# Performance work log

Measured on AMD Instinct MI355X. Metric: run time of the kernel, lower is better.

Reference implementation:

```python
import jax, jax.numpy as jnp
import numpy as np

LN_EPS = 1e-5


def setup_inputs() -> dict:
    key = jax.random.key(0)
    ks = jax.random.split(key, 6)
    n_nodes, mem_dim = 500000, 256
    n_upd, msg_dim = 65536, 512
    return {
        "unique_node_ids": jnp.arange(n_upd, dtype=jnp.int64) if jax.config.jax_enable_x64 else jnp.arange(n_upd, dtype=jnp.int32),
        "unique_messages": jax.random.normal(ks[0], (n_upd, msg_dim), dtype=jnp.float32),
        "timestamps": jax.random.uniform(ks[1], (n_upd,), dtype=jnp.float32),
        "memory": jax.random.normal(ks[2], (n_nodes, mem_dim), dtype=jnp.float32),
        "last_update": jnp.zeros((n_nodes,), dtype=jnp.float32),
        "W_ih": jax.random.normal(ks[3], (3 * mem_dim, msg_dim), dtype=jnp.float32) * (1.0 / np.sqrt(msg_dim)),
        "W_hh": jax.random.normal(ks[4], (3 * mem_dim, mem_dim), dtype=jnp.float32) * (1.0 / np.sqrt(mem_dim)),
        "b_ih": jnp.zeros((3 * mem_dim,), dtype=jnp.float32),
        "b_hh": jnp.zeros((3 * mem_dim,), dtype=jnp.float32),
        "ln_gamma": jnp.ones((mem_dim,), dtype=jnp.float32),
        "ln_beta": jnp.zeros((mem_dim,), dtype=jnp.float32),
    }


def _gru_cell(x, h, W_ih, W_hh, b_ih, b_hh):
    # torch.nn.GRUCell math
    gi = x @ W_ih.T + b_ih          # [N, 3H]
    gh = h @ W_hh.T + b_hh          # [N, 3H]
    i_r, i_z, i_n = jnp.split(gi, 3, axis=-1)
    h_r, h_z, h_n = jnp.split(gh, 3, axis=-1)
    r = jax.nn.sigmoid(i_r + h_r)
    z = jax.nn.sigmoid(i_z + h_z)
    n = jnp.tanh(i_n + r * h_n)
    return (1.0 - z) * n + z * h


def _layer_norm(x, gamma, beta):
    mu = jnp.mean(x, axis=-1, keepdims=True)
    var = jnp.mean(jnp.square(x - mu), axis=-1, keepdims=True)
    return (x - mu) * jax.lax.rsqrt(var + LN_EPS) * gamma + beta


def reference(unique_node_ids, unique_messages, timestamps, memory, last_update,
              W_ih, W_hh, b_ih, b_hh, ln_gamma, ln_beta):
    # gather memory rows for the nodes being updated
    h = memory[unique_node_ids]                      # [N, H]
    new_h = _gru_cell(unique_messages, h, W_ih, W_hh, b_ih, b_hh)
    new_h = _layer_norm(new_h, ln_gamma, ln_beta)
    # scatter updated rows back (get_updated_memory semantics: pure copy)
    updated_memory = memory.at[unique_node_ids].set(new_h)
    updated_last_update = last_update.at[unique_node_ids].set(timestamps)
    return updated_memory, updated_last_update
```

## Files before the change

kernel.cpp:

```cpp
#include <hip/hip_runtime.h>
#include <hip/hip_bf16.h>

typedef float  f32x4 __attribute__((ext_vector_type(4)));
typedef short  s16x8 __attribute__((ext_vector_type(8)));

#define MEMH   256
#define MSGD   512
#define G3     768
#define W_IH_ELEMS (G3*MSGD)
#define W_HH_ELEMS (G3*MEMH)
#define W_TOT_ELEMS (W_IH_ELEMS + W_HH_ELEMS)
#define W_BYTES    ((size_t)W_TOT_ELEMS * 2)

#define BM     64
#define NTHR   1024
#define AH_OFF 0
#define AM_OFF 32768
#define O_OFF  32768
#define LDS_BYTES (32768 + 66560)

static __device__ __forceinline__ short f2bf(float x) {
    __hip_bfloat16 b = __float2bfloat16(x);
    return __builtin_bit_cast(short, b);
}
static __device__ __forceinline__ float bf2f(short s) {
    unsigned int u = ((unsigned int)(unsigned short)s) << 16;
    return __builtin_bit_cast(float, u);
}
static __device__ __forceinline__ float sigf(float x) {
    return 1.f / (1.f + __expf(-x));
}
static __device__ __forceinline__ float tanh_fast(float x) {
    float e = __expf(-2.f * fabsf(x));
    float t = (1.f - e) / (1.f + e);
    return copysignf(t, x);
}
static __device__ __forceinline__ f32x4 ntload4(const float* p) {
    return __builtin_nontemporal_load((const f32x4*)p);
}
static __device__ __forceinline__ void ntstore4(float* p, f32x4 v) {
    __builtin_nontemporal_store(v, (f32x4*)p);
}

__global__ void smu_copy_kernel(const float* __restrict__ mem,
                                const float* __restrict__ lu,
                                float* __restrict__ out_mem,
                                float* __restrict__ out_lu,
                                long n_mem4, long n_lu4) {
    long i = (long)blockIdx.x * blockDim.x + threadIdx.x;
    long stride = (long)gridDim.x * blockDim.x;
    long total = n_mem4 + n_lu4;
    for (; i < total; i += stride) {
        if (i < n_mem4) ntstore4(out_mem + i * 4, ntload4(mem + i * 4));
        else {
            long j = (i - n_mem4) * 4;
            ntstore4(out_lu + j, ntload4(lu + j));
        }
    }
}

__global__ void smu_cvtw_kernel(const float* __restrict__ wih,
                                const float* __restrict__ whh,
                                short* __restrict__ o) {
    int i = blockIdx.x * blockDim.x + threadIdx.x;
    if (i >= W_TOT_ELEMS) return;
    if (i < W_IH_ELEMS) {
        int f = i >> 9, r = i & 511, l = r >> 3, e = r & 7;
        int t = f >> 4, k = f & 15;
        int row = t * 16 + (l & 15), col = k * 32 + (l >> 4) * 8 + e;
        o[i] = f2bf(wih[row * MSGD + col]);
    } else {
        int j = i - W_IH_ELEMS;
        int f = j >> 9, r = j & 511, l = r >> 3, e = r & 7;
        int t = f >> 3, k = f & 7;
        int row = t * 16 + (l & 15), col = k * 32 + (l >> 4) * 8 + e;
        o[i] = f2bf(whh[row * MEMH + col]);
    }
}

__global__ void smu_bits_kernel(const int* __restrict__ ids,
                                unsigned* __restrict__ bm, int n) {
    int i = blockIdx.x * blockDim.x + threadIdx.x;
    if (i < n) {
        int id = ids[i];
        atomicOr(&bm[id >> 5], 1u << (id & 31));
    }
}

template<bool USE_WS>
static __device__ __forceinline__ s16x8 load_b(const float* __restrict__ Wf,
                                               const short* __restrict__ Wb,
                                               int t, int k, int ldk, int nkt, int lane) {
    if constexpr (USE_WS) {
        return *(const s16x8*)(Wb + ((size_t)(t * nkt + k) << 9) + lane * 8);
    } else {
        int row = t * 16 + (lane & 15);
        int col = k * 32 + (lane >> 4) * 8;
        f32x4 x = *(const f32x4*)(Wf + (size_t)row * ldk + col);
        f32x4 y = *(const f32x4*)(Wf + (size_t)row * ldk + col + 4);
        s16x8 s;
        s[0]=f2bf(x[0]); s[1]=f2bf(x[1]); s[2]=f2bf(x[2]); s[3]=f2bf(x[3]);
        s[4]=f2bf(y[0]); s[5]=f2bf(y[1]); s[6]=f2bf(y[2]); s[7]=f2bf(y[3]);
        return s;
    }
}

#define CP_LOAD(BUF, s) do { if constexpr (FUSED) {                                   \
    const int lo_ = (s) * 2;                                                          \
    const long o0_ = (long)w * 48 + lo_;                                              \
    const long r0_ = crow_base + o0_;                                                 \
    cpf_##BUF##0 = (o0_ < cpslab) && (r0_ < n_nodes) && !((cpwin >> lo_) & 1);        \
    cpf_##BUF##1 = (o0_ + 1 < cpslab) && (r0_ + 1 < n_nodes) && !((cpwin >> (lo_ + 1)) & 1); \
    if (cpf_##BUF##0) cpv_##BUF##0 = ntload4(memory + r0_ * MEMH + (lane << 2));      \
    if (cpf_##BUF##1) cpv_##BUF##1 = ntload4(memory + (r0_ + 1) * MEMH + (lane << 2));\
  } } while (0)

#define CP_STORE(BUF, s) do { if constexpr (FUSED) {                                  \
    const long r0_ = crow_base + (long)w * 48 + (s) * 2;                              \
    if (cpf_##BUF##0) ntstore4(out_mem + r0_ * MEMH + (lane << 2), cpv_##BUF##0);     \
    if (cpf_##BUF##1) ntstore4(out_mem + (r0_ + 1) * MEMH + (lane << 2), cpv_##BUF##1);\
    cpf_##BUF##0 = false; cpf_##BUF##1 = false;                                       \
  } } while (0)

template<bool USE_WS, bool FUSED>
__global__ __launch_bounds__(NTHR, 1)
void smu_gru_kernel(const int*   __restrict__ ids,
                    const float* __restrict__ msg,
                    const float* __restrict__ ts,
                    const float* __restrict__ memory,
                    const float* __restrict__ lu,
                    const float* __restrict__ W_ih,
                    const float* __restrict__ W_hh,
                    const float* __restrict__ b_ih,
                    const float* __restrict__ b_hh,
                    const float* __restrict__ gamma,
                    const float* __restrict__ beta,
                    const short* __restrict__ wsw,
                    const unsigned* __restrict__ bm,
                    float* __restrict__ out_mem,
                    float* __restrict__ out_lu,
                    long n_nodes, long cpslab) {
    __shared__ __align__(16) unsigned char lds[LDS_BYTES];
    const int tid  = threadIdx.x;
    const int bid  = blockIdx.x;
    const long base = (long)bid * BM;
    const long crow_base = (long)bid * cpslab;

    {
        const float* src = msg + base * MSGD;
        #pragma unroll
        for (int it = 0; it < 4; ++it) {
            int u = tid + NTHR * it;
            int row = u >> 6;
            f32x4 a = ntload4(src + u * 8);
            f32x4 b = ntload4(src + u * 8 + 4);
            s16x8 s;
            s[0]=f2bf(a[0]); s[1]=f2bf(a[1]); s[2]=f2bf(a[2]); s[3]=f2bf(a[3]);
            s[4]=f2bf(b[0]); s[5]=f2bf(b[1]); s[6]=f2bf(b[2]); s[7]=f2bf(b[3]);
            int byte = AM_OFF + ((u * 16) ^ ((row & 7) << 4));
            *(s16x8*)(lds + byte) = s;
        }
        #pragma unroll
        for (int it = 0; it < 2; ++it) {
            int u = tid + NTHR * it;
            int row = u >> 5;
            int c8  = u & 31;
            int id  = ids[base + row];
            const float* hs = memory + (size_t)id * MEMH + c8 * 8;
            f32x4 a = ntload4(hs);
            f32x4 b = ntload4(hs + 4);
            s16x8 s;
            s[0]=f2bf(a[0]); s[1]=f2bf(a[1]); s[2]=f2bf(a[2]); s[3]=f2bf(a[3]);
            s[4]=f2bf(b[0]); s[5]=f2bf(b[1]); s[6]=f2bf(b[2]); s[7]=f2bf(b[3]);
            int byte = AH_OFF + ((u * 16) ^ ((row & 7) << 4));
            *(s16x8*)(lds + byte) = s;
        }
    }
    __syncthreads();

    const int lane = tid & 63;
    const int w    = tid >> 6;
    const int lr   = lane & 15;
    const int lk8  = (lane >> 4) * 8;
    const int sw   = (lr & 7) << 4;
    const short* Wi = wsw;
    const short* Wh = wsw + W_IH_ELEMS;

    f32x4 cpv_A0, cpv_A1, cpv_B0, cpv_B1;
    bool  cpf_A0 = false, cpf_A1 = false, cpf_B0 = false, cpf_B1 = false;
    unsigned long long cpwin = 0;
    if constexpr (FUSED) {
        long start = crow_base + (long)w * 48;
        long wi = start >> 5;
        int  off = (int)(start & 31);
        unsigned b0 = bm[wi], b1 = bm[wi + 1], b2 = bm[wi + 2];
        unsigned long long lo64 = ((unsigned long long)b1 << 32) | b0;
        cpwin = lo64 >> off;
        if (off) cpwin |= ((unsigned long long)b2) << (64 - off);
    }

    f32x4 acc[4][3] = {};
    f32x4 accn[4]   = {};

    {
        s16x8 b[2][3];
        #pragma unroll
        for (int i = 0; i < 3; ++i) b[0][i] = load_b<USE_WS>(W_ih, Wi, w + 16*i, 0, MSGD, 16, lane);
        #pragma unroll
        for (int i = 0; i < 3; ++i) b[1][i] = load_b<USE_WS>(W_ih, Wi, w + 16*i, 1, MSGD, 16, lane);
        #pragma unroll
        for (int k = 0; k < 16; ++k) {
            if ((k & 1) == 0) { CP_STORE(A, k - 2); CP_LOAD(A, k); }
            else              { CP_STORE(B, k - 2); CP_LOAD(B, k); }
            const int cb = (k * 32 + lk8) * 2;
            #pragma unroll
            for (int m = 0; m < 4; ++m) {
                s16x8 a = *(const s16x8*)(lds + AM_OFF + (((m*16 + lr) * 1024 + cb) ^ sw));
                #pragma unroll
                for (int i = 0; i < 3; ++i)
                    acc[m][i] = __builtin_amdgcn_mfma_f32_16x16x32_bf16(a, b[k & 1][i], acc[m][i], 0, 0, 0);
            }
            if (k < 14) {
                #pragma unroll
                for (int i = 0; i < 3; ++i)
                    b[k & 1][i] = load_b<USE_WS>(W_ih, Wi, w + 16*i, k + 2, MSGD, 16, lane);
            }
        }
    }
    {
        s16x8 b[2][3];
        #pragma unroll
        for (int i = 0; i < 3; ++i) b[0][i] = load_b<USE_WS>(W_hh, Wh, w + 16*i, 0, MEMH, 8, lane);
        #pragma unroll
        for (int i = 0; i < 3; ++i) b[1][i] = load_b<USE_WS>(W_hh, Wh, w + 16*i, 1, MEMH, 8, lane);
        #pragma unroll
        for (int k = 0; k < 8; ++k) {
            if ((k & 1) == 0) { CP_STORE(A, 14 + k); CP_LOAD(A, 16 + k); }
            else              { CP_STORE(B, 14 + k); CP_LOAD(B, 16 + k); }
            const int cb = (k * 32 + lk8) * 2;
            #pragma unroll
            for (int m = 0; m < 4; ++m) {
                s16x8 a = *(const s16x8*)(lds + AH_OFF + (((m*16 + lr) * 512 + cb) ^ sw));
                acc[m][0] = __builtin_amdgcn_mfma_f32_16x16x32_bf16(a, b[k & 1][0], acc[m][0], 0, 0, 0);
                acc[m][1] = __builtin_amdgcn_mfma_f32_16x16x32_bf16(a, b[k & 1][1], acc[m][1], 0, 0, 0);
                accn[m]   = __builtin_amdgcn_mfma_f32_16x16x32_bf16(a, b[k & 1][2], accn[m],   0, 0, 0);
            }
            if (k < 6) {
                #pragma unroll
                for (int i = 0; i < 3; ++i)
                    b[k & 1][i] = load_b<USE_WS>(W_hh, Wh, w + 16*i, k + 2, MEMH, 8, lane);
            }
        }
    }
    CP_STORE(A, 22);
    CP_STORE(B, 23);

    __syncthreads();

    {
        const int lq = (lane >> 4) * 4;
        const int j  = w * 16 + lr;
        const float br = b_ih[j]       + b_hh[j];
        const float bz = b_ih[256 + j] + b_hh[256 + j];
        const float bihn = b_ih[512 + j], bhhn = b_hh[512 + j];
        #pragma unroll
        for (int m = 0; m < 4; ++m) {
            #pragma unroll
            for (int q = 0; q < 4; ++q) {
                int row = m * 16 + lq + q;
                float r = sigf(acc[m][0][q] + br);
                float z = sigf(acc[m][1][q] + bz);
                float n = tanh_fast(acc[m][2][q] + bihn + r * (accn[m][q] + bhhn));
                float hv = bf2f(*(const short*)(lds + AH_OFF + ((row * 512 + j * 2) ^ ((row & 7) << 4))));
                float o = (1.f - z) * n + z * hv;
                *(float*)(lds + O_OFF + (row * 260 + j) * 4) = o;
            }
        }
    }
    __syncthreads();

    #pragma unroll
    for (int rr = 0; rr < 4; ++rr) {
        int row = w * 4 + rr;
        f32x4 x = *(const f32x4*)(lds + O_OFF + (row * 260 + lane * 4) * 4);
        float s1 = x[0] + x[1] + x[2] + x[3];
        float s2 = x[0]*x[0] + x[1]*x[1] + x[2]*x[2] + x[3]*x[3];
        #pragma unroll
        for (int mm = 32; mm > 0; mm >>= 1) {
            s1 += __shfl_xor(s1, mm);
            s2 += __shfl_xor(s2, mm);
        }
        float mu  = s1 * (1.f / 256.f);
        float var = fmaxf(s2 * (1.f / 256.f) - mu * mu, 0.f);
        float inv = rsqrtf(var + 1e-5f);
        f32x4 g  = *(const f32x4*)(gamma + lane * 4);
        f32x4 be = *(const f32x4*)(beta  + lane * 4);
        int id = ids[base + row];
        f32x4 y;
        #pragma unroll
        for (int c = 0; c < 4; ++c) y[c] = (x[c] - mu) * inv * g[c] + be[c];
        ntstore4(out_mem + (size_t)id * MEMH + lane * 4, y);
        if (lane == 0) __builtin_nontemporal_store(ts[base + row], out_lu + id);
    }

    if constexpr (FUSED) {
        for (long o = 768 + w; o < cpslab; o += 16) {
            long row = crow_base + o;
            if (row < n_nodes && !((bm[row >> 5] >> (row & 31)) & 1u)) {
                f32x4 v = ntload4(memory + row * MEMH + (lane << 2));
                ntstore4(out_mem + row * MEMH + (lane << 2), v);
            }
        }
        for (long i = (long)bid * NTHR + tid; i < n_nodes; i += (long)gridDim.x * NTHR) {
            if (!((bm[i >> 5] >> (i & 31)) & 1u)) {
                float v = __builtin_nontemporal_load(lu + i);
                __builtin_nontemporal_store(v, out_lu + i);
            }
        }
    }
}

extern "C" void kernel_launch(void* const* d_in, const int* in_sizes, int n_in,
                              void* d_out, int out_size, void* d_ws, size_t ws_size,
                              hipStream_t stream) {
    (void)n_in; (void)out_size;
    const int*   ids = (const int*)  d_in[0];
    const float* msg = (const float*)d_in[1];
    const float* ts  = (const float*)d_in[2];
    const float* mem = (const float*)d_in[3];
    const float* lu  = (const float*)d_in[4];
    const float* Wih = (const float*)d_in[5];
    const float* Whh = (const float*)d_in[6];
    const float* bih = (const float*)d_in[7];
    const float* bhh = (const float*)d_in[8];
    const float* gam = (const float*)d_in[9];
    const float* bet = (const float*)d_in[10];

    const int  n_upd   = in_sizes[0];
    const long n_nodes = (long)in_sizes[3] / MEMH;

    float* out_mem = (float*)d_out;
    float* out_lu  = out_mem + (size_t)n_nodes * MEMH;

    const size_t bm_words = (size_t)((n_nodes + 31) / 32);
    const size_t bm_bytes_pad = bm_words * 4 + 16;
    const bool ws_w  = (d_ws != nullptr) && (ws_size >= W_BYTES);
    const bool ws_bm = (d_ws != nullptr) && (ws_size >= W_BYTES + bm_bytes_pad);

    short*    wsw = (short*)d_ws;
    unsigned* bm  = (unsigned*)((char*)d_ws + W_BYTES);

    if (ws_w) {
        smu_cvtw_kernel<<<(W_TOT_ELEMS + 255) / 256, 256, 0, stream>>>(Wih, Whh, wsw);
    }
    if (ws_bm) {
        (void)hipMemsetAsync(bm, 0, bm_bytes_pad, stream);
        smu_bits_kernel<<<(n_upd + 255) / 256, 256, 0, stream>>>(ids, bm, n_upd);
    }

    const int  grid   = n_upd / BM;
    const long cpslab = (n_nodes + grid - 1) / grid;

    if (ws_bm) {
        smu_gru_kernel<true, true><<<grid, NTHR, 0, stream>>>(
            ids, msg, ts, mem, lu, Wih, Whh, bih, bhh, gam, bet,
            wsw, bm, out_mem, out_lu, n_nodes, cpslab);
    } else {
        long n_mem4 = n_nodes * (MEMH / 4);
        long n_lu4  = n_nodes / 4;
        smu_copy_kernel<<<2048, 256, 0, stream>>>(mem, lu, out_mem, out_lu,
                                                  n_mem4, n_lu4);
        if (ws_w) {
            smu_gru_kernel<true, false><<<grid, NTHR, 0, stream>>>(
                ids, msg, ts, mem, lu, Wih, Whh, bih, bhh, gam, bet,
                wsw, nullptr, out_mem, out_lu, n_nodes, cpslab);
        } else {
            smu_gru_kernel<false, false><<<grid, NTHR, 0, stream>>>(
                ids, msg, ts, mem, lu, Wih, Whh, bih, bhh, gam, bet,
                nullptr, nullptr, out_mem, out_lu, n_nodes, cpslab);
        }
    }
}
```

Before: 386.3 us.

## Split bitmap-skipping memory copy out of GRU kernel into separate launch

Removes the copy of untouched memory rows that was interleaved with the MFMA loops inside the GRU kernel. That copy now runs in a dedicated grid-stride kernel, launched after the GRU kernel, which skips rows flagged in the update bitmap and issues four independent loads before storing. This simplifies the GRU kernel and may lower its register pressure. The cost is losing the overlap between compute and the roughly 500 MB streaming copy, plus one extra launch.

```diff
diff --git a/kernel.cpp b/kernel.cpp
--- a/kernel.cpp
+++ b/kernel.cpp
@@ -55,6 +55,54 @@
         else {
             long j = (i - n_mem4) * 4;
             ntstore4(out_lu + j, ntload4(lu + j));
+        }
+    }
+}
+
+__global__ __launch_bounds__(256)
+void smu_copy_skip_kernel(const float* __restrict__ mem,
+                          const float* __restrict__ lu,
+                          const unsigned* __restrict__ bm,
+                          float* __restrict__ out_mem,
+                          float* __restrict__ out_lu,
+                          long n_nodes) {
+    const long nu = n_nodes * (MEMH / 4);
+    const long stride = (long)gridDim.x * blockDim.x;
+    const long i0 = (long)blockIdx.x * blockDim.x + threadIdx.x;
+
+    for (long i = i0; i < nu; i += stride * 4) {
+        long  u0 = i, u1 = i + stride, u2 = i + stride * 2, u3 = i + stride * 3;
+        f32x4 v0, v1, v2, v3;
+        bool  f0 = false, f1 = false, f2 = false, f3 = false;
+        {
+            long r = u0 >> 6;
+            f0 = !((bm[r >> 5] >> (r & 31)) & 1u);
+            if (f0) v0 = ntload4(mem + u0 * 4);
+        }
+        if (u1 < nu) {
+            long r = u1 >> 6;
+            f1 = !((bm[r >> 5] >> (r & 31)) & 1u);
+            if (f1) v1 = ntload4(mem + u1 * 4);
+        }
+        if (u2 < nu) {
+            long r = u2 >> 6;
+            f2 = !((bm[r >> 5] >> (r & 31)) & 1u);
+            if (f2) v2 = ntload4(mem + u2 * 4);
+        }
+        if (u3 < nu) {
+            long r = u3 >> 6;
+            f3 = !((bm[r >> 5] >> (r & 31)) & 1u);
+            if (f3) v3 = ntload4(mem + u3 * 4);
+        }
+        if (f0) ntstore4(out_mem + u0 * 4, v0);
+        if (f1) ntstore4(out_mem + u1 * 4, v1);
+        if (f2) ntstore4(out_mem + u2 * 4, v2);
+        if (f3) ntstore4(out_mem + u3 * 4, v3);
+    }
+    for (long i = i0; i < n_nodes; i += stride) {
+        if (!((bm[i >> 5] >> (i & 31)) & 1u)) {
+            float v = __builtin_nontemporal_load(lu + i);
+            __builtin_nontemporal_store(v, out_lu + i);
         }
     }
 }
@@ -105,30 +153,12 @@
     }
 }
 
-#define CP_LOAD(BUF, s) do { if constexpr (FUSED) {                                   \
-    const int lo_ = (s) * 2;                                                          \
-    const long o0_ = (long)w * 48 + lo_;                                              \
-    const long r0_ = crow_base + o0_;                                                 \
-    cpf_##BUF##0 = (o0_ < cpslab) && (r0_ < n_nodes) && !((cpwin >> lo_) & 1);        \
-    cpf_##BUF##1 = (o0_ + 1 < cpslab) && (r0_ + 1 < n_nodes) && !((cpwin >> (lo_ + 1)) & 1); \
-    if (cpf_##BUF##0) cpv_##BUF##0 = ntload4(memory + r0_ * MEMH + (lane << 2));      \
-    if (cpf_##BUF##1) cpv_##BUF##1 = ntload4(memory + (r0_ + 1) * MEMH + (lane << 2));\
-  } } while (0)
-
-#define CP_STORE(BUF, s) do { if constexpr (FUSED) {                                  \
-    const long r0_ = crow_base + (long)w * 48 + (s) * 2;                              \
-    if (cpf_##BUF##0) ntstore4(out_mem + r0_ * MEMH + (lane << 2), cpv_##BUF##0);     \
-    if (cpf_##BUF##1) ntstore4(out_mem + (r0_ + 1) * MEMH + (lane << 2), cpv_##BUF##1);\
-    cpf_##BUF##0 = false; cpf_##BUF##1 = false;                                       \
-  } } while (0)
-
-template<bool USE_WS, bool FUSED>
+template<bool USE_WS>
 __global__ __launch_bounds__(NTHR, 1)
 void smu_gru_kernel(const int*   __restrict__ ids,
                     const float* __restrict__ msg,
                     const float* __restrict__ ts,
                     const float* __restrict__ memory,
-                    const float* __restrict__ lu,
                     const float* __restrict__ W_ih,
                     const float* __restrict__ W_hh,
                     const float* __restrict__ b_ih,
@@ -136,15 +166,12 @@
                     const float* __restrict__ gamma,
                     const float* __restrict__ beta,
                     const short* __restrict__ wsw,
-                    const unsigned* __restrict__ bm,
                     float* __restrict__ out_mem,
-                    float* __restrict__ out_lu,
-                    long n_nodes, long cpslab) {
+                    float* __restrict__ out_lu) {
     __shared__ __align__(16) unsigned char lds[LDS_BYTES];
     const int tid  = threadIdx.x;
     const int bid  = blockIdx.x;
     const long base = (long)bid * BM;
-    const long crow_base = (long)bid * cpslab;
 
     {
         const float* src = msg + base * MSGD;
@@ -186,19 +213,6 @@
     const short* Wi = wsw;
     const short* Wh = wsw + W_IH_ELEMS;
 
-    f32x4 cpv_A0, cpv_A1, cpv_B0, cpv_B1;
-    bool  cpf_A0 = false, cpf_A1 = false, cpf_B0 = false, cpf_B1 = false;
-    unsigned long long cpwin = 0;
-    if constexpr (FUSED) {
-        long start = crow_base + (long)w * 48;
-        long wi = start >> 5;
-        int  off = (int)(start & 31);
-        unsigned b0 = bm[wi], b1 = bm[wi + 1], b2 = bm[wi + 2];
-        unsigned long long lo64 = ((unsigned long long)b1 << 32) | b0;
-        cpwin = lo64 >> off;
-        if (off) cpwin |= ((unsigned long long)b2) << (64 - off);
-    }
-
     f32x4 acc[4][3] = {};
     f32x4 accn[4]   = {};
 
@@ -210,8 +224,6 @@
         for (int i = 0; i < 3; ++i) b[1][i] = load_b<USE_WS>(W_ih, Wi, w + 16*i, 1, MSGD, 16, lane);
         #pragma unroll
         for (int k = 0; k < 16; ++k) {
-            if ((k & 1) == 0) { CP_STORE(A, k - 2); CP_LOAD(A, k); }
-            else              { CP_STORE(B, k - 2); CP_LOAD(B, k); }
             const int cb = (k * 32 + lk8) * 2;
             #pragma unroll
             for (int m = 0; m < 4; ++m) {
@@ -235,8 +247,6 @@
         for (int i = 0; i < 3; ++i) b[1][i] = load_b<USE_WS>(W_hh, Wh, w + 16*i, 1, MEMH, 8, lane);
         #pragma unroll
         for (int k = 0; k < 8; ++k) {
-            if ((k & 1) == 0) { CP_STORE(A, 14 + k); CP_LOAD(A, 16 + k); }
-            else              { CP_STORE(B, 14 + k); CP_LOAD(B, 16 + k); }
             const int cb = (k * 32 + lk8) * 2;
             #pragma unroll
             for (int m = 0; m < 4; ++m) {
@@ -252,8 +262,6 @@
             }
         }
     }
-    CP_STORE(A, 22);
-    CP_STORE(B, 23);
 
     __syncthreads();
 
@@ -301,22 +309,6 @@
         for (int c = 0; c < 4; ++c) y[c] = (x[c] - mu) * inv * g[c] + be[c];
         ntstore4(out_mem + (size_t)id * MEMH + lane * 4, y);
         if (lane == 0) __builtin_nontemporal_store(ts[base + row], out_lu + id);
-    }
-
-    if constexpr (FUSED) {
-        for (long o = 768 + w; o < cpslab; o += 16) {
-            long row = crow_base + o;
-            if (row < n_nodes && !((bm[row >> 5] >> (row & 31)) & 1u)) {
-                f32x4 v = ntload4(memory + row * MEMH + (lane << 2));
-                ntstore4(out_mem + row * MEMH + (lane << 2), v);
-            }
-        }
-        for (long i = (long)bid * NTHR + tid; i < n_nodes; i += (long)gridDim.x * NTHR) {
-            if (!((bm[i >> 5] >> (i & 31)) & 1u)) {
-                float v = __builtin_nontemporal_load(lu + i);
-                __builtin_nontemporal_store(v, out_lu + i);
-            }
-        }
     }
 }
 
@@ -350,34 +342,28 @@
     short*    wsw = (short*)d_ws;
     unsigned* bm  = (unsigned*)((char*)d_ws + W_BYTES);
 
+    const int grid = n_upd / BM;
+
     if (ws_w) {
         smu_cvtw_kernel<<<(W_TOT_ELEMS + 255) / 256, 256, 0, stream>>>(Wih, Whh, wsw);
     }
+
     if (ws_bm) {
         (void)hipMemsetAsync(bm, 0, bm_bytes_pad, stream);
         smu_bits_kernel<<<(n_upd + 255) / 256, 256, 0, stream>>>(ids, bm, n_upd);
-    }
-
-    const int  grid   = n_upd / BM;
-    const long cpslab = (n_nodes + grid - 1) / grid;
-
-    if (ws_bm) {
-        smu_gru_kernel<true, true><<<grid, NTHR, 0, stream>>>(
-            ids, msg, ts, mem, lu, Wih, Whh, bih, bhh, gam, bet,
-            wsw, bm, out_mem, out_lu, n_nodes, cpslab);
+        smu_gru_kernel<true><<<grid, NTHR, 0, stream>>>(
+            ids, msg, ts, mem, Wih, Whh, bih, bhh, gam, bet, wsw, out_mem, out_lu);
+        smu_copy_skip_kernel<<<2048, 256, 0, stream>>>(mem, lu, bm, out_mem, out_lu, n_nodes);
     } else {
         long n_mem4 = n_nodes * (MEMH / 4);
         long n_lu4  = n_nodes / 4;
-        smu_copy_kernel<<<2048, 256, 0, stream>>>(mem, lu, out_mem, out_lu,
-                                                  n_mem4, n_lu4);
+        smu_copy_kernel<<<2048, 256, 0, stream>>>(mem, lu, out_mem, out_lu, n_mem4, n_lu4);
         if (ws_w) {
-            smu_gru_kernel<true, false><<<grid, NTHR, 0, stream>>>(
-                ids, msg, ts, mem, lu, Wih, Whh, bih, bhh, gam, bet,
-                wsw, nullptr, out_mem, out_lu, n_nodes, cpslab);
+            smu_gru_kernel<true><<<grid, NTHR, 0, stream>>>(
+                ids, msg, ts, mem, Wih, Whh, bih, bhh, gam, bet, wsw, out_mem, out_lu);
         } else {
-            smu_gru_kernel<false, false><<<grid, NTHR, 0, stream>>>(
-                ids, msg, ts, mem, lu, Wih, Whh, bih, bhh, gam, bet,
-                nullptr, nullptr, out_mem, out_lu, n_nodes, cpslab);
-        }
-    }
-}
+            smu_gru_kernel<false><<<grid, NTHR, 0, stream>>>(
+                ids, msg, ts, mem, Wih, Whh, bih, bhh, gam, bet, nullptr, out_mem, out_lu);
+        }
+    }
+}
```

New measurement: 350.8 us. 9.2% less time.
